# Kernel optimization log

Measured on AMD Instinct MI355X. Metric: run time of the kernel, lower is better.

Reference implementation:

```python
import math
import jax, jax.numpy as jnp
import numpy as np

B, H, I, O = 8192, 2048, 1024, 512
EPS = 1e-6
T_INF = 10000.0


def next_spike(v, eta):
    sqrt_eta = jnp.sqrt(jnp.abs(eta) + EPS)
    v_safe = v + EPS * jnp.sign(v) + 0.5 * EPS * jnp.sign(v + EPS)
    pi = jnp.asarray(math.pi, v.dtype)
    case_zero = jnp.where(v > 0, 1.0 / v_safe, T_INF)
    case_neg = jnp.where(
        v > sqrt_eta,
        jnp.arctanh(jnp.clip(sqrt_eta / v_safe, -1 + EPS, 1 - EPS)) / sqrt_eta,
        T_INF,
    )
    case_pos = jnp.mod(jnp.arctan(sqrt_eta / v_safe), pi) / sqrt_eta
    return jnp.where(eta == 0, case_zero, jnp.where(eta < 0, case_neg, case_pos))


def update_potential(v, eta, dt):
    sqrt_eta = jnp.sqrt(jnp.abs(eta) + EPS)
    th = jnp.tanh(sqrt_eta * dt)
    ta = jnp.tan(sqrt_eta * dt)
    case_zero = v / (1 - dt * v)
    case_neg = (v - sqrt_eta * th) / (1 - th * v / sqrt_eta)
    case_pos = (v + sqrt_eta * ta) / (1 - ta * v / sqrt_eta)
    v_new = jnp.where(eta == 0, case_zero, jnp.where(eta < 0, case_neg, case_pos))
    return jnp.clip(v_new, -1e25, 1e25)


def setup_inputs():
    key = jax.random.key(0)
    ks = jax.random.split(key, 10)
    return dict(
        input_spike=jax.random.normal(ks[0], (B, H), jnp.float32) * 0.1,
        input_current=jax.random.normal(ks[1], (B, I), jnp.float32),
        v=jax.random.normal(ks[2], (B, H), jnp.float32),
        t=jnp.zeros((B,), jnp.float32),
        w_i2h=jax.random.normal(ks[3], (H, I), jnp.float32) / math.sqrt(I),
        b_i2h=jax.random.normal(ks[4], (H,), jnp.float32) / math.sqrt(I),
        w_h2h=jax.random.normal(ks[5], (H, H), jnp.float32) / math.sqrt(H),
        b_h2h=jax.random.normal(ks[6], (H,), jnp.float32),
        w_h2o=jax.random.normal(ks[7], (O, H), jnp.float32) / math.sqrt(H),
        b_h2o=jax.random.normal(ks[8], (O,), jnp.float32) / math.sqrt(H),
        syn_delay=jnp.float32(0.1),
        vmin=jnp.float32(-10.0),
        vmax=jnp.float32(10.0),
    )


def reference(input_spike, input_current, v, t, w_i2h, b_i2h, w_h2h, b_h2h,
              w_h2o, b_h2o, syn_delay, vmin, vmax):
    # v <- v + spikes; eta = h2h.bias + i2h(current)
    v = v + input_spike                                   # [B,H]
    eta = b_h2h + input_current @ w_i2h.T + b_i2h         # [B,H]
    dt_all = next_spike(v, eta)                           # [B,H]
    min_dt = jnp.min(dt_all, axis=1)                      # [B]
    k = jnp.argmin(dt_all, axis=1)                        # [B] int
    v = update_potential(v, eta, (min_dt + syn_delay)[:, None])
    v = v + jnp.take(w_h2h.T, k, axis=0)                  # recurrent column gather
    t = t + min_dt + syn_delay
    output_spike = jnp.take(w_h2o.T, k, axis=0)           # [B,O]
    output_potential = jnp.clip(v, vmin, vmax) @ w_h2o.T + b_h2o  # [B,O]
    return (output_spike, output_potential, v, t, min_dt, k)
```

## Files before the change

kernel.cpp:

```cpp
#include <hip/hip_runtime.h>
#include <math.h>

#define B_SZ 8192
#define H_SZ 2048
#define I_SZ 1024
#define O_SZ 512

typedef double v4d __attribute__((ext_vector_type(4)));
typedef float v4f __attribute__((ext_vector_type(4)));
typedef short v8bf __attribute__((ext_vector_type(8)));


__device__ __forceinline__ float signf_(float x) {
    return (x > 0.f) ? 1.f : ((x < 0.f) ? -1.f : 0.f);
}

__device__ __forceinline__ float next_spike_f32(float v, float eta) {
#pragma clang fp contract(off)
    const float EPSf = 1e-6f;
    const float HEPSf = (float)(0.5 * 1e-6);
    const float T_INF = 10000.f;
    const float PI_F = (float)3.14159265358979323846;
    float ae = fabsf(eta) + EPSf;
    float se = (float)sqrt((double)ae);
    float s1 = signf_(v);
    float t1 = EPSf * s1;
    float va = v + t1;
    float vpe = v + EPSf;
    float s2 = signf_(vpe);
    float t2 = HEPSf * s2;
    float vs = va + t2;
    if (eta == 0.f) {
        if (v > 0.f) return 1.f / vs;
        return T_INF;
    }
    if (eta < 0.f) {
        if (v > se) {
            float r = se / vs;
            const float lo = (float)(-1.0 + 1e-6);
            const float hi = (float)(1.0 - 1e-6);
            r = fminf(fmaxf(r, lo), hi);
            float at = atanhf(r);
            return at / se;
        }
        return T_INF;
    }
    float q = se / vs;
    float a = atanf(q);
    if (a < 0.f) a = a + PI_F;
    return a / se;
}

__device__ __forceinline__ float update_pot_f32(float v, float eta, float dt) {
#pragma clang fp contract(off)
    const float EPSf = 1e-6f;
    float ae = fabsf(eta) + EPSf;
    float se = (float)sqrt((double)ae);
    float r;
    if (eta == 0.f) {
        float t1 = dt * v;
        float den = 1.f - t1;
        r = v / den;
    } else if (eta < 0.f) {
        float x = se * dt;
        float th = tanhf(x);
        float t1 = se * th;
        float num = v - t1;
        float t2 = th * v;
        float t3 = t2 / se;
        float den = 1.f - t3;
        r = num / den;
    } else {
        float x = se * dt;
        float ta = tanf(x);
        float t1 = se * ta;
        float num = v + t1;
        float t2 = ta * v;
        float t3 = t2 / se;
        float den = 1.f - t3;
        r = num / den;
    }
    const float HI = (float)1e25;
    r = r < -HI ? -HI : (r > HI ? HI : r);
    return r;
}


__global__ __launch_bounds__(256) void transpose_kernel(const float* __restrict__ in,
                                                        float* __restrict__ out,
                                                        int R, int C) {
    __shared__ float tile[32][33];
    int bx = blockIdx.x * 32;
    int by = blockIdx.y * 32;
    int tx = threadIdx.x;
    int ty = threadIdx.y;
#pragma unroll
    for (int i = ty; i < 32; i += 8)
        tile[i][tx] = in[(size_t)(by + i) * C + bx + tx];
    __syncthreads();
#pragma unroll
    for (int i = ty; i < 32; i += 8)
        out[(size_t)(bx + i) * R + by + tx] = tile[tx][i];
}


#define EBK 32

__device__ __forceinline__ void stage_tile_dma(
    const float* __restrict__ A, const float* __restrict__ Bm,
    float (*Asb)[32], float (*Bsb)[32],
    int row0, int col0, int k0, int tid) {
    const int wid = tid >> 6;
    const int lane = tid & 63;
    const int sr8 = lane >> 3;
    const int ksw = ((lane & 7) ^ sr8) << 2;
#pragma unroll
    for (int p = 0; p < 2; ++p) {
        const int rbase = p * 64 + wid * 8;
        const float* ga = A + (size_t)(row0 + rbase + sr8) * I_SZ + k0 + ksw;
        const float* gb = Bm + (size_t)(col0 + rbase + sr8) * I_SZ + k0 + ksw;
        float* la = &Asb[rbase][0];
        float* lb = &Bsb[rbase][0];
        __builtin_amdgcn_global_load_lds(
            (const __attribute__((address_space(1))) void*)ga,
            (__attribute__((address_space(3))) void*)la, 16, 0, 0);
        __builtin_amdgcn_global_load_lds(
            (const __attribute__((address_space(1))) void*)gb,
            (__attribute__((address_space(3))) void*)lb, 16, 0, 0);
    }
}

__global__ __launch_bounds__(512) void gemm_eta_mfma_f64(
    const float* __restrict__ A,
    const float* __restrict__ Bm,
    const float* __restrict__ b_i2h, const float* __restrict__ b_h2h,
    float* __restrict__ C) {
    __shared__ float As[2][128][32];
    __shared__ float Bs[2][128][32];
    const int tid = threadIdx.x;
    const int row0 = blockIdx.y * 128;
    const int col0 = blockIdx.x * 128;
    const int wid = tid >> 6;
    const int lane = tid & 63;
    const int wrow = wid >> 1;
    const int wcol = wid & 1;
    const int lr = lane & 15;
    const int lk = lane >> 4;
    const int csw = (lr & 7) << 2;

    v4d acc[2][4];
#pragma unroll
    for (int i = 0; i < 2; ++i)
#pragma unroll
        for (int j = 0; j < 4; ++j) acc[i][j] = (v4d){0.0, 0.0, 0.0, 0.0};

    stage_tile_dma(A, Bm, As[0], Bs[0], row0, col0, 0, tid);
    __syncthreads();

    int cur = 0;
    for (int k0 = 0; k0 < I_SZ; k0 += EBK) {
        int knext = k0 + EBK;
        if (knext < I_SZ)
            stage_tile_dma(A, Bm, As[cur ^ 1], Bs[cur ^ 1], row0, col0, knext, tid);
#pragma unroll
        for (int ks = 0; ks < EBK / 4; ++ks) {
            int kk = ks * 4 + lk;
            int kks = kk ^ csw;
            double a[2], b[4];
#pragma unroll
            for (int i = 0; i < 2; ++i)
                a[i] = (double)As[cur][wrow * 32 + i * 16 + lr][kks];
#pragma unroll
            for (int j = 0; j < 4; ++j)
                b[j] = (double)Bs[cur][wcol * 64 + j * 16 + lr][kks];
#pragma unroll
            for (int i = 0; i < 2; ++i)
#pragma unroll
                for (int j = 0; j < 4; ++j)
                    acc[i][j] = __builtin_amdgcn_mfma_f64_16x16x4f64(
                        a[i], b[j], acc[i][j], 0, 0, 0);
        }
        __syncthreads();
        cur ^= 1;
    }
    {
#pragma clang fp contract(off)
#pragma unroll
        for (int i = 0; i < 2; ++i) {
#pragma unroll
            for (int j = 0; j < 4; ++j) {
                int gcol = col0 + wcol * 64 + j * 16 + lr;
#pragma unroll
                for (int q = 0; q < 4; ++q) {
                    int grow = row0 + wrow * 32 + i * 16 + q * 4 + lk;
                    float m32 = (float)acc[i][j][q];
                    float s = b_h2h[gcol] + m32;
                    s = s + b_i2h[gcol];
                    C[(size_t)grow * H_SZ + gcol] = s;
                }
            }
        }
    }
}


__global__ __launch_bounds__(256) void spike_min_kernel(
    const float* __restrict__ v_in, const float* __restrict__ spike,
    const float* __restrict__ eta, const float* __restrict__ t_in,
    const float* __restrict__ syn_p,
    float* __restrict__ t_out, float* __restrict__ mdt_out,
    float* __restrict__ kf_out, int* __restrict__ kidx) {
#pragma clang fp contract(off)
    const int b = blockIdx.x;
    const int tid = threadIdx.x;
    const size_t base = (size_t)b * H_SZ;
    unsigned long long best = 0xFFFFFFFFFFFFFFFFull;
    for (int h = tid; h < H_SZ; h += 256) {
        float vv = v_in[base + h] + spike[base + h];
        float dt = next_spike_f32(vv, eta[base + h]);
        unsigned long long p =
            ((unsigned long long)__float_as_uint(dt) << 32) | (unsigned)h;
        best = (p < best) ? p : best;
    }
#pragma unroll
    for (int off = 1; off < 64; off <<= 1) {
        unsigned long long o = __shfl_xor(best, off);
        best = (o < best) ? o : best;
    }
    __shared__ unsigned long long s[4];
    if ((tid & 63) == 0) s[tid >> 6] = best;
    __syncthreads();
    if (tid == 0) {
        best = s[0];
#pragma unroll
        for (int w = 1; w < 4; ++w)
            if (s[w] < best) best = s[w];
        float mdt = __uint_as_float((unsigned)(best >> 32));
        int k = (int)(best & 0xFFFFFFFFu);
        mdt_out[b] = mdt;
        kf_out[b] = (float)k;
        kidx[b] = k;
        float tt = t_in[b] + mdt;
        tt = tt + (*syn_p);
        t_out[b] = tt;
    }
}


__global__ __launch_bounds__(256) void update_v_kernel(
    const float* __restrict__ v_in, const float* __restrict__ spike,
    const float* __restrict__ eta, const float* __restrict__ mdt,
    const int* __restrict__ kidx, const float* __restrict__ whhT,
    const float* __restrict__ syn_p, float* __restrict__ v_out) {
#pragma clang fp contract(off)
    size_t i4 = ((size_t)blockIdx.x * 256 + threadIdx.x) * 4;
    if (i4 >= (size_t)B_SZ * H_SZ) return;
    int b = (int)(i4 >> 11);
    int h = (int)(i4 & (H_SZ - 1));
    float dt = mdt[b] + (*syn_p);
    int k = kidx[b];
    float4 v4 = *reinterpret_cast<const float4*>(v_in + i4);
    float4 s4 = *reinterpret_cast<const float4*>(spike + i4);
    float4 e4 = *reinterpret_cast<const float4*>(eta + i4);
    float4 w4 = *reinterpret_cast<const float4*>(whhT + (size_t)k * H_SZ + h);
    float4 r;
    r.x = update_pot_f32(v4.x + s4.x, e4.x, dt) + w4.x;
    r.y = update_pot_f32(v4.y + s4.y, e4.y, dt) + w4.y;
    r.z = update_pot_f32(v4.z + s4.z, e4.z, dt) + w4.z;
    r.w = update_pot_f32(v4.w + s4.w, e4.w, dt) + w4.w;
    *reinterpret_cast<float4*>(v_out + i4) = r;
}


__global__ __launch_bounds__(256) void out_spike_kernel(
    const int* __restrict__ kidx, const float* __restrict__ whoT,
    float* __restrict__ out0) {
    size_t i4 = ((size_t)blockIdx.x * 256 + threadIdx.x) * 4;
    if (i4 >= (size_t)B_SZ * O_SZ) return;
    int b = (int)(i4 >> 9);
    int o = (int)(i4 & (O_SZ - 1));
    int k = kidx[b];
    float4 w = *reinterpret_cast<const float4*>(whoT + (size_t)k * O_SZ + o);
    *reinterpret_cast<float4*>(out0 + i4) = w;
}


#define OBK 32

__device__ __forceinline__ unsigned short bf16_rn(float x) {
    unsigned u = __float_as_uint(x);
    unsigned r = (u + 0x7fffu + ((u >> 16) & 1u)) >> 16;
    return (unsigned short)r;
}

__global__ __launch_bounds__(256) void gemm_out1_bf16x3(
    const float* __restrict__ A,
    const float* __restrict__ Bm,
    const float* __restrict__ bias0, float* __restrict__ C,
    const float* __restrict__ vminp, const float* __restrict__ vmaxp) {
    __shared__ unsigned short Ah[64][40], Al[64][40];
    __shared__ unsigned short Bh[64][40], Bl[64][40];
    const int tid = threadIdx.x;
    const int row0 = blockIdx.y * 64;
    const int col0 = blockIdx.x * 64;
    const float vmin = *vminp, vmax = *vmaxp;
    const int wid = tid >> 6, lane = tid & 63;
    const int wrow = wid >> 1, wcol = wid & 1;
    const int lr = lane & 15;
    const int lg = lane >> 4;
    const int srow = tid >> 2;
    const int scol = (tid & 3) * 8;

    v4f acc[2][2];
#pragma unroll
    for (int i = 0; i < 2; ++i)
#pragma unroll
        for (int j = 0; j < 2; ++j) acc[i][j] = (v4f){0.f, 0.f, 0.f, 0.f};

    for (int k0 = 0; k0 < H_SZ; k0 += OBK) {
#pragma unroll
        for (int p = 0; p < 2; ++p) {
            float4 a4 = *reinterpret_cast<const float4*>(
                A + (size_t)(row0 + srow) * H_SZ + k0 + scol + p * 4);
            float4 b4 = *reinterpret_cast<const float4*>(
                Bm + (size_t)(col0 + srow) * H_SZ + k0 + scol + p * 4);
            float av[4] = {fminf(fmaxf(a4.x, vmin), vmax),
                           fminf(fmaxf(a4.y, vmin), vmax),
                           fminf(fmaxf(a4.z, vmin), vmax),
                           fminf(fmaxf(a4.w, vmin), vmax)};
            float bv[4] = {b4.x, b4.y, b4.z, b4.w};
#pragma unroll
            for (int e = 0; e < 4; ++e) {
                int cc = scol + p * 4 + e;
                unsigned short ha = bf16_rn(av[e]);
                float hfa = __uint_as_float((unsigned)ha << 16);
                Ah[srow][cc] = ha;
                Al[srow][cc] = bf16_rn(av[e] - hfa);
                unsigned short hb = bf16_rn(bv[e]);
                float hfb = __uint_as_float((unsigned)hb << 16);
                Bh[srow][cc] = hb;
                Bl[srow][cc] = bf16_rn(bv[e] - hfb);
            }
        }
        __syncthreads();
        v8bf ah[2], al[2], bh[2], bl[2];
#pragma unroll
        for (int i = 0; i < 2; ++i) {
            ah[i] = *reinterpret_cast<const v8bf*>(&Ah[wrow * 32 + i * 16 + lr][lg * 8]);
            al[i] = *reinterpret_cast<const v8bf*>(&Al[wrow * 32 + i * 16 + lr][lg * 8]);
        }
#pragma unroll
        for (int j = 0; j < 2; ++j) {
            bh[j] = *reinterpret_cast<const v8bf*>(&Bh[wcol * 32 + j * 16 + lr][lg * 8]);
            bl[j] = *reinterpret_cast<const v8bf*>(&Bl[wcol * 32 + j * 16 + lr][lg * 8]);
        }
#pragma unroll
        for (int i = 0; i < 2; ++i)
#pragma unroll
            for (int j = 0; j < 2; ++j) {
                acc[i][j] = __builtin_amdgcn_mfma_f32_16x16x32_bf16(
                    ah[i], bh[j], acc[i][j], 0, 0, 0);
                acc[i][j] = __builtin_amdgcn_mfma_f32_16x16x32_bf16(
                    ah[i], bl[j], acc[i][j], 0, 0, 0);
                acc[i][j] = __builtin_amdgcn_mfma_f32_16x16x32_bf16(
                    al[i], bh[j], acc[i][j], 0, 0, 0);
            }
        __syncthreads();
    }
#pragma unroll
    for (int i = 0; i < 2; ++i)
#pragma unroll
        for (int j = 0; j < 2; ++j) {
            int gcol = col0 + wcol * 32 + j * 16 + lr;
            float bb = bias0[gcol];
#pragma unroll
            for (int q = 0; q < 4; ++q) {
                int grow = row0 + wrow * 32 + i * 16 + lg * 4 + q;
                C[(size_t)grow * O_SZ + gcol] = acc[i][j][q] + bb;
            }
        }
}


extern "C" void kernel_launch(void* const* d_in, const int* in_sizes, int n_in,
                              void* d_out, int out_size, void* d_ws, size_t ws_size,
                              hipStream_t stream) {
    const float* in_spike = (const float*)d_in[0];
    const float* in_cur   = (const float*)d_in[1];
    const float* v_in     = (const float*)d_in[2];
    const float* t_in     = (const float*)d_in[3];
    const float* w_i2h    = (const float*)d_in[4];
    const float* b_i2h    = (const float*)d_in[5];
    const float* w_h2h    = (const float*)d_in[6];
    const float* b_h2h    = (const float*)d_in[7];
    const float* w_h2o    = (const float*)d_in[8];
    const float* b_h2o    = (const float*)d_in[9];
    const float* syn_p    = (const float*)d_in[10];
    const float* vmin_p   = (const float*)d_in[11];
    const float* vmax_p   = (const float*)d_in[12];

    float* out0    = (float*)d_out;
    float* out1    = out0 + (size_t)B_SZ * O_SZ;
    float* out_v   = out1 + (size_t)B_SZ * O_SZ;
    float* out_t   = out_v + (size_t)B_SZ * H_SZ;
    float* out_mdt = out_t + B_SZ;
    float* out_kf  = out_mdt + B_SZ;

    float* eta  = (float*)d_ws;
    int*   kidx = (int*)(eta + (size_t)B_SZ * H_SZ);
    float* whhT = (float*)(kidx + B_SZ);
    float* whoT = whhT + (size_t)H_SZ * H_SZ;

    dim3 tb(32, 8);
    transpose_kernel<<<dim3(H_SZ / 32, H_SZ / 32), tb, 0, stream>>>(w_h2h, whhT,
                                                                    H_SZ, H_SZ);
    transpose_kernel<<<dim3(H_SZ / 32, O_SZ / 32), tb, 0, stream>>>(w_h2o, whoT,
                                                                    O_SZ, H_SZ);

    gemm_eta_mfma_f64<<<dim3(H_SZ / 128, B_SZ / 128), 512, 0, stream>>>(
        in_cur, w_i2h, b_i2h, b_h2h, eta);

    spike_min_kernel<<<B_SZ, 256, 0, stream>>>(v_in, in_spike, eta, t_in, syn_p,
                                               out_t, out_mdt, out_kf, kidx);

    update_v_kernel<<<(B_SZ * H_SZ / 4 + 255) / 256, 256, 0, stream>>>(
        v_in, in_spike, eta, out_mdt, kidx, whhT, syn_p, out_v);

    out_spike_kernel<<<(B_SZ * O_SZ / 4 + 255) / 256, 256, 0, stream>>>(kidx, whoT,
                                                                        out0);

    gemm_out1_bf16x3<<<dim3(O_SZ / 64, B_SZ / 64), 256, 0, stream>>>(
        out_v, w_h2o, b_h2o, out1, vmin_p, vmax_p);
}
```

Measured before the change: 789.6 us.

## Fuse spike argmin, potential update, and output spike gather into one row kernel

```diff
diff --git a/kernel.cpp b/kernel.cpp
--- a/kernel.cpp
+++ b/kernel.cpp
@@ -204,20 +204,37 @@
 }
 
 
-__global__ __launch_bounds__(256) void spike_min_kernel(
+__global__ __launch_bounds__(256) void fused_row_kernel(
     const float* __restrict__ v_in, const float* __restrict__ spike,
     const float* __restrict__ eta, const float* __restrict__ t_in,
     const float* __restrict__ syn_p,
+    const float* __restrict__ whhT, const float* __restrict__ whoT,
     float* __restrict__ t_out, float* __restrict__ mdt_out,
-    float* __restrict__ kf_out, int* __restrict__ kidx) {
+    float* __restrict__ kf_out, int* __restrict__ kidx_out,
+    float* __restrict__ v_out, float* __restrict__ out0) {
 #pragma clang fp contract(off)
     const int b = blockIdx.x;
     const int tid = threadIdx.x;
     const size_t base = (size_t)b * H_SZ;
+    const int h0 = tid * 4;
+    const int h1 = tid * 4 + 1024;
+
+    float4 v0 = *reinterpret_cast<const float4*>(v_in + base + h0);
+    float4 v1 = *reinterpret_cast<const float4*>(v_in + base + h1);
+    float4 s0 = *reinterpret_cast<const float4*>(spike + base + h0);
+    float4 s1 = *reinterpret_cast<const float4*>(spike + base + h1);
+    float4 e0 = *reinterpret_cast<const float4*>(eta + base + h0);
+    float4 e1 = *reinterpret_cast<const float4*>(eta + base + h1);
+
+    float vv[8] = {v0.x + s0.x, v0.y + s0.y, v0.z + s0.z, v0.w + s0.w,
+                   v1.x + s1.x, v1.y + s1.y, v1.z + s1.z, v1.w + s1.w};
+    float ee[8] = {e0.x, e0.y, e0.z, e0.w, e1.x, e1.y, e1.z, e1.w};
+
     unsigned long long best = 0xFFFFFFFFFFFFFFFFull;
-    for (int h = tid; h < H_SZ; h += 256) {
-        float vv = v_in[base + h] + spike[base + h];
-        float dt = next_spike_f32(vv, eta[base + h]);
+#pragma unroll
+    for (int q = 0; q < 8; ++q) {
+        int h = (q < 4) ? (h0 + q) : (h1 + q - 4);
+        float dt = next_spike_f32(vv[q], ee[q]);
         unsigned long long p =
             ((unsigned long long)__float_as_uint(dt) << 32) | (unsigned)h;
         best = (p < best) ? p : best;
@@ -230,58 +247,42 @@
     __shared__ unsigned long long s[4];
     if ((tid & 63) == 0) s[tid >> 6] = best;
     __syncthreads();
+    best = s[0];
+#pragma unroll
+    for (int w = 1; w < 4; ++w)
+        if (s[w] < best) best = s[w];
+    float mdt = __uint_as_float((unsigned)(best >> 32));
+    int k = (int)(best & 0xFFFFFFFFu);
+    float syn = *syn_p;
+
     if (tid == 0) {
-        best = s[0];
-#pragma unroll
-        for (int w = 1; w < 4; ++w)
-            if (s[w] < best) best = s[w];
-        float mdt = __uint_as_float((unsigned)(best >> 32));
-        int k = (int)(best & 0xFFFFFFFFu);
         mdt_out[b] = mdt;
         kf_out[b] = (float)k;
-        kidx[b] = k;
+        kidx_out[b] = k;
         float tt = t_in[b] + mdt;
-        tt = tt + (*syn_p);
+        tt = tt + syn;
         t_out[b] = tt;
     }
-}
-
-
-__global__ __launch_bounds__(256) void update_v_kernel(
-    const float* __restrict__ v_in, const float* __restrict__ spike,
-    const float* __restrict__ eta, const float* __restrict__ mdt,
-    const int* __restrict__ kidx, const float* __restrict__ whhT,
-    const float* __restrict__ syn_p, float* __restrict__ v_out) {
-#pragma clang fp contract(off)
-    size_t i4 = ((size_t)blockIdx.x * 256 + threadIdx.x) * 4;
-    if (i4 >= (size_t)B_SZ * H_SZ) return;
-    int b = (int)(i4 >> 11);
-    int h = (int)(i4 & (H_SZ - 1));
-    float dt = mdt[b] + (*syn_p);
-    int k = kidx[b];
-    float4 v4 = *reinterpret_cast<const float4*>(v_in + i4);
-    float4 s4 = *reinterpret_cast<const float4*>(spike + i4);
-    float4 e4 = *reinterpret_cast<const float4*>(eta + i4);
-    float4 w4 = *reinterpret_cast<const float4*>(whhT + (size_t)k * H_SZ + h);
-    float4 r;
-    r.x = update_pot_f32(v4.x + s4.x, e4.x, dt) + w4.x;
-    r.y = update_pot_f32(v4.y + s4.y, e4.y, dt) + w4.y;
-    r.z = update_pot_f32(v4.z + s4.z, e4.z, dt) + w4.z;
-    r.w = update_pot_f32(v4.w + s4.w, e4.w, dt) + w4.w;
-    *reinterpret_cast<float4*>(v_out + i4) = r;
-}
-
-
-__global__ __launch_bounds__(256) void out_spike_kernel(
-    const int* __restrict__ kidx, const float* __restrict__ whoT,
-    float* __restrict__ out0) {
-    size_t i4 = ((size_t)blockIdx.x * 256 + threadIdx.x) * 4;
-    if (i4 >= (size_t)B_SZ * O_SZ) return;
-    int b = (int)(i4 >> 9);
-    int o = (int)(i4 & (O_SZ - 1));
-    int k = kidx[b];
-    float4 w = *reinterpret_cast<const float4*>(whoT + (size_t)k * O_SZ + o);
-    *reinterpret_cast<float4*>(out0 + i4) = w;
+
+    float dtq = mdt + syn;
+    float4 w0 = *reinterpret_cast<const float4*>(whhT + (size_t)k * H_SZ + h0);
+    float4 w1 = *reinterpret_cast<const float4*>(whhT + (size_t)k * H_SZ + h1);
+    float4 r0, r1;
+    r0.x = update_pot_f32(vv[0], ee[0], dtq) + w0.x;
+    r0.y = update_pot_f32(vv[1], ee[1], dtq) + w0.y;
+    r0.z = update_pot_f32(vv[2], ee[2], dtq) + w0.z;
+    r0.w = update_pot_f32(vv[3], ee[3], dtq) + w0.w;
+    r1.x = update_pot_f32(vv[4], ee[4], dtq) + w1.x;
+    r1.y = update_pot_f32(vv[5], ee[5], dtq) + w1.y;
+    r1.z = update_pot_f32(vv[6], ee[6], dtq) + w1.z;
+    r1.w = update_pot_f32(vv[7], ee[7], dtq) + w1.w;
+    *reinterpret_cast<float4*>(v_out + base + h0) = r0;
+    *reinterpret_cast<float4*>(v_out + base + h1) = r1;
+
+    if (tid < 128) {
+        float4 w = *reinterpret_cast<const float4*>(whoT + (size_t)k * O_SZ + tid * 4);
+        *reinterpret_cast<float4*>(out0 + (size_t)b * O_SZ + tid * 4) = w;
+    }
 }
 
 
@@ -420,14 +421,9 @@
     gemm_eta_mfma_f64<<<dim3(H_SZ / 128, B_SZ / 128), 512, 0, stream>>>(
         in_cur, w_i2h, b_i2h, b_h2h, eta);
 
-    spike_min_kernel<<<B_SZ, 256, 0, stream>>>(v_in, in_spike, eta, t_in, syn_p,
-                                               out_t, out_mdt, out_kf, kidx);
-
-    update_v_kernel<<<(B_SZ * H_SZ / 4 + 255) / 256, 256, 0, stream>>>(
-        v_in, in_spike, eta, out_mdt, kidx, whhT, syn_p, out_v);
-
-    out_spike_kernel<<<(B_SZ * O_SZ / 4 + 255) / 256, 256, 0, stream>>>(kidx, whoT,
-                                                                        out0);
+    fused_row_kernel<<<B_SZ, 256, 0, stream>>>(
+        v_in, in_spike, eta, t_in, syn_p, whhT, whoT,
+        out_t, out_mdt, out_kf, kidx, out_v, out0);
 
     gemm_out1_bf16x3<<<dim3(O_SZ / 64, B_SZ / 64), 256, 0, stream>>>(
         out_v, w_h2o, b_h2o, out1, vmin_p, vmax_p);
```

Result: faster. 770.5 us (-2.4%).
